# Optimization experiments

Measured on AMD Instinct MI355X. Metric: run time of the kernel, lower is better.

The kernel has to match this reference:

```python
import jax, jax.numpy as jnp
import numpy as np

E, D_IN, H1, H2 = 10, 784, 256, 64


def setup_inputs() -> dict:
    key = jax.random.key(0)
    ks = jax.random.split(key, 11)
    s = lambda fan_in: 1.0 / np.sqrt(fan_in)
    return {
        "x": jax.random.normal(ks[0], (65536, D_IN), dtype=jnp.float32),
        # stacked expert weights (E experts of Linear layers)
        "W1": jax.random.uniform(ks[1], (E, D_IN, H1), jnp.float32, -s(D_IN), s(D_IN)),
        "b1": jax.random.uniform(ks[2], (E, H1), jnp.float32, -s(D_IN), s(D_IN)),
        "W2": jax.random.uniform(ks[3], (E, H1, H2), jnp.float32, -s(H1), s(H1)),
        "b2": jax.random.uniform(ks[4], (E, H2), jnp.float32, -s(H1), s(H1)),
        "W3": jax.random.uniform(ks[5], (E, H2), jnp.float32, -s(H2), s(H2)),  # [E,64,1] squeezed
        "b3": jax.random.uniform(ks[6], (E,), jnp.float32, -s(H2), s(H2)),
        # gate: 784 -> 256 -> E
        "Wg1": jax.random.uniform(ks[7], (D_IN, H1), jnp.float32, -s(D_IN), s(D_IN)),
        "bg1": jax.random.uniform(ks[8], (H1,), jnp.float32, -s(D_IN), s(D_IN)),
        "Wg2": jax.random.uniform(ks[9], (H1, E), jnp.float32, -s(H1), s(H1)),
        "bg2": jax.random.uniform(ks[10], (E,), jnp.float32, -s(H1), s(H1)),
    }


def reference(x, W1, b1, W2, b2, W3, b3, Wg1, bg1, Wg2, bg2):
    # dense all-experts MLP stack, batched over experts as grouped GEMMs
    h = jax.nn.relu(jnp.einsum("bi,eih->beh", x, W1) + b1)        # [B,E,256]
    h = jax.nn.relu(jnp.einsum("beh,ehk->bek", h, W2) + b2)        # [B,E,64]
    expert_outputs = jnp.einsum("bek,ek->be", h, W3) + b3          # [B,E]
    g = jax.nn.relu(x @ Wg1 + bg1)
    gate_scores = jax.nn.softmax(g @ Wg2 + bg2, axis=-1)           # [B,E]
    output = gate_scores * expert_outputs                          # [B,E]
    return (output, gate_scores, expert_outputs)
```

## Files before the change

kernel.cpp:

```cpp
#include <hip/hip_runtime.h>
#include <hip/hip_bf16.h>
#include <stdint.h>

#define BTOT   65536
#define DIN    784
#define NH1    256
#define NH2    64
#define NEXP   10
#define BM     256
#define NKS1   25

#define SLOT(s)   (lds + (s) * 32768)
#define EXPL_OFF  131072
#define B2S_OFF   141312
#define W3S_OFF   143872
#define B3S_OFF   146432
#define BG2S_OFF  146496
#define LDS_TOTAL 146560

typedef short s16x8  __attribute__((ext_vector_type(8)));
typedef float f32x4  __attribute__((ext_vector_type(4)));
typedef float f32x16 __attribute__((ext_vector_type(16)));

__device__ __forceinline__ short bf16b(float v) {
    __bf16 b = (__bf16)v;
    return __builtin_bit_cast(short, b);
}

__device__ __forceinline__ void g2l16(const void* g, void* l) {
    __builtin_amdgcn_global_load_lds(
        (const __attribute__((address_space(1))) unsigned char*)g,
        (__attribute__((address_space(3))) unsigned char*)l, 16, 0, 0);
}

__global__ void prep_w1(const float* __restrict__ W1, const float* __restrict__ b1,
                        const float* __restrict__ Wg1, const float* __restrict__ bg1,
                        __bf16* __restrict__ dst) {
    int t = blockIdx.x * 256 + threadIdx.x;
    int lane = t & 63;
    int kh = (t >> 6) & 1;
    int nb = (t >> 7) & 7;
    int r  = t >> 10;
    int ks = r % 25, e = r / 25;
    int n  = nb * 32 + (lane & 31);
    int k0 = ks * 32 + kh * 16 + (lane >> 5) * 8;
    const float* src  = (e < NEXP) ? (W1 + (size_t)e * DIN * NH1) : Wg1;
    const float* bias = (e < NEXP) ? (b1 + e * NH1) : bg1;
    s16x8 o;
    #pragma unroll
    for (int j = 0; j < 8; ++j) {
        int k = k0 + j;
        float v = (k < DIN) ? src[(size_t)k * NH1 + n]
                            : ((k == DIN) ? bias[n] : 0.f);
        o[j] = bf16b(v);
    }
    *(s16x8*)((short*)dst + (size_t)t * 8) = o;
}

__global__ void prep_w2(const float* __restrict__ W2, __bf16* __restrict__ dst) {
    int t = blockIdx.x * 256 + threadIdx.x;
    int lane = t & 63;
    int kh = (t >> 6) & 1;
    int ks = (t >> 7) & 7;
    int jb = (t >> 10) & 1;
    int e  = t >> 11;
    int n  = jb * 32 + (lane & 31);
    int k0 = ks * 32 + kh * 16 + (lane >> 5) * 8;
    s16x8 o;
    #pragma unroll
    for (int j = 0; j < 8; ++j)
        o[j] = bf16b(W2[((size_t)e * NH1 + k0 + j) * NH2 + n]);
    *(s16x8*)((short*)dst + (size_t)t * 8) = o;
}

__global__ void prep_wg2(const float* __restrict__ Wg2, __bf16* __restrict__ dst) {
    int t = blockIdx.x * 256 + threadIdx.x;
    if (t >= 1024) return;
    int lane = t & 63;
    int kh = (t >> 6) & 1;
    int ks = t >> 7;
    int n  = lane & 31;
    int k0 = ks * 32 + kh * 16 + (lane >> 5) * 8;
    s16x8 o;
    #pragma unroll
    for (int j = 0; j < 8; ++j)
        o[j] = bf16b((n < NEXP) ? Wg2[(size_t)(k0 + j) * NEXP + n] : 0.f);
    *(s16x8*)((short*)dst + (size_t)t * 8) = o;
}

__global__ void prep_x(const float* __restrict__ x, __bf16* __restrict__ dst) {
    __shared__ short xl[32 * 800];
    const int rb = blockIdx.x >> 3, mq = blockIdx.x & 7;
    const int tid = threadIdx.x;
    const float* xg = x + ((size_t)rb * 256 + mq * 32) * DIN;
    #pragma unroll 4
    for (int i = 0; i < 25; ++i) {
        int idx = tid + i * 256;
        if (idx < 6272) {
            int r = idx / 196, c = (idx % 196) * 4;
            float4 v = *(const float4*)(xg + (size_t)r * DIN + c);
            uint2 w; short* p = (short*)&w;
            p[0] = bf16b(v.x); p[1] = bf16b(v.y);
            p[2] = bf16b(v.z); p[3] = bf16b(v.w);
            *(uint2*)(xl + r * 800 + c) = w;
        }
    }
    for (int i = tid; i < 32 * 16; i += 256) {
        int r = i >> 4, k = DIN + (i & 15);
        xl[r * 800 + k] = (k == DIN) ? bf16b(1.f) : (short)0;
    }
    __syncthreads();
    #pragma unroll 2
    for (int i = 0; i < 13; ++i) {
        int idx = tid + i * 256;
        if (idx < 3200) {
            int row = idx & 31, c8 = idx >> 5;
            int ks = c8 >> 2, rem = c8 & 3;
            int kh = rem >> 1, hw = rem & 1;
            s16x8 v = *(const s16x8*)(xl + row * 800 + ks * 32 + kh * 16 + hw * 8);
            *(s16x8*)((char*)dst + (((size_t)(rb * 25 + ks) * 8 + mq) * 2048)
                      + kh * 1024 + hw * 512 + row * 16) = v;
        }
    }
}

#define STAGE(S, E, KS) {                                                     \
        const char* xs_ = xtc + ((size_t)(KS) << 14) + tid * 16;              \
        char* xd_ = SLOT(S) + tid * 16;                                       \
        g2l16(xs_, xd_); g2l16(xs_ + 8192, xd_ + 8192);                       \
        const char* ws_ = w1c + (((size_t)(E) * 25 + (KS)) << 14) + tid * 16; \
        char* wd_ = SLOT(S) + 16384 + tid * 16;                               \
        g2l16(ws_, wd_); g2l16(ws_ + 8192, wd_ + 8192); }

#define COMPUTE(S) {                                                          \
        const char* ab = SLOT(S) + mw * 4096 + lane * 16;                     \
        const char* wb = SLOT(S) + 16384 + nw * 8192 + lane * 16;             \
        s16x8 xv[2][2], wv[4][2];                                             \
        _Pragma("unroll") for (int mt = 0; mt < 2; ++mt)                      \
            _Pragma("unroll") for (int kh = 0; kh < 2; ++kh)                  \
                xv[mt][kh] = *(const s16x8*)(ab + (mt * 2 + kh) * 1024);      \
        _Pragma("unroll") for (int nt = 0; nt < 4; ++nt)                      \
            _Pragma("unroll") for (int kh = 0; kh < 2; ++kh)                  \
                wv[nt][kh] = *(const s16x8*)(wb + (nt * 2 + kh) * 1024);      \
        _Pragma("unroll") for (int kh = 0; kh < 2; ++kh)                      \
            _Pragma("unroll") for (int nt = 0; nt < 4; ++nt)                  \
                _Pragma("unroll") for (int mt = 0; mt < 2; ++mt)              \
                    acc[nt][mt] = __builtin_amdgcn_mfma_f32_32x32x16_bf16(    \
                        wv[nt][kh], xv[mt][kh], acc[nt][mt], 0, 0, 0); }

#define RING_SYNC(VN) {                                                       \
        asm volatile("s_waitcnt vmcnt(" #VN ")" ::: "memory");                \
        __builtin_amdgcn_s_barrier();                                         \
        asm volatile("" ::: "memory"); }

#define BODY(S, KS) {                                                         \
        RING_SYNC(8)                                                          \
        COMPUTE(S)                                                            \
        STAGE(((S) + 3) & 3, e, (KS) + 3) }

__global__ void __launch_bounds__(512)
__attribute__((amdgpu_waves_per_eu(2, 2)))
moe_fused(const __bf16* __restrict__ xt, const float* __restrict__ b2g,
          const float* __restrict__ W3, const float* __restrict__ b3,
          const float* __restrict__ bg2, const __bf16* __restrict__ w1t,
          const __bf16* __restrict__ w2t, const __bf16* __restrict__ wg2t,
          float* __restrict__ out)
{
    extern __shared__ char lds[];
    char*  hb   = lds;
    float* expl = (float*)(lds + EXPL_OFF);
    float* b2s  = (float*)(lds + B2S_OFF);
    float* w3s  = (float*)(lds + W3S_OFF);
    float* b3s  = (float*)(lds + B3S_OFF);
    float* bg2s = (float*)(lds + BG2S_OFF);

    const int tid  = threadIdx.x;
    const int lane = tid & 63;
    const int wave = tid >> 6;
    const int rl   = lane & 31;
    const int hi   = lane >> 5;
    const int mw   = wave >> 1;
    const int nw   = wave & 1;
    const int row0 = blockIdx.x * BM;
    const char* w1c = (const char*)w1t;
    const char* w2c = (const char*)w2t;
    const char* wgc = (const char*)wg2t;
    const char* xtc = (const char*)xt + ((size_t)blockIdx.x * 25 << 14);

    for (int i = tid; i < NEXP * NH2; i += 512) { b2s[i] = b2g[i]; w3s[i] = W3[i]; }
    if (tid < NEXP) { b3s[tid] = b3[tid]; bg2s[tid] = bg2[tid]; }
    __syncthreads();

    f32x16 acc[4][2];

    #pragma unroll 1
    for (int e = 0; e <= NEXP; ++e) {
        #pragma unroll
        for (int nt = 0; nt < 4; ++nt)
            #pragma unroll
            for (int mt = 0; mt < 2; ++mt)
                #pragma unroll
                for (int q = 0; q < 16; ++q) acc[nt][mt][q] = 0.f;

        STAGE(0, e, 0)
        STAGE(1, e, 1)
        STAGE(2, e, 2)

        #pragma unroll 1
        for (int T = 0; T < 5; ++T) {
            const int k4 = 4 * T;
            BODY(0, k4)
            BODY(1, k4 + 1)
            BODY(2, k4 + 2)
            BODY(3, k4 + 3)
        }
        BODY(0, 20)
        BODY(1, 21)
        RING_SYNC(8)  COMPUTE(2)
        RING_SYNC(4)  COMPUTE(3)
        RING_SYNC(0)  COMPUTE(0)
        __syncthreads();

        #pragma unroll
        for (int mt = 0; mt < 2; ++mt)
            #pragma unroll
            for (int nt = 0; nt < 4; ++nt)
                #pragma unroll
                for (int q = 0; q < 4; ++q) {
                    uint2 wvv; short* p = (short*)&wvv;
                    #pragma unroll
                    for (int r2 = 0; r2 < 4; ++r2)
                        p[r2] = bf16b(fmaxf(acc[nt][mt][q * 4 + r2], 0.f));
                    *(uint2*)(hb + (((mw * 2 + mt) * 8 + (nw * 4 + nt)) * 2
                                    + (q >> 1)) * 1024
                                 + (q & 1) * 512 + rl * 16 + hi * 8) = wvv;
                }
        __syncthreads();

        if (e < NEXP) {
            f32x16 acc2[2];
            #pragma unroll
            for (int q = 0; q < 16; ++q) { acc2[0][q] = 0.f; acc2[1][q] = 0.f; }
            #pragma unroll
            for (int jb = 0; jb < 2; ++jb)
                #pragma unroll
                for (int k2 = 0; k2 < 8; ++k2)
                    #pragma unroll
                    for (int kh = 0; kh < 2; ++kh) {
                        s16x8 hf = *(const s16x8*)(hb + ((wave * 8 + k2) * 2 + kh) * 1024
                                                   + lane * 16);
                        s16x8 wf = *(const s16x8*)(w2c
                            + ((((size_t)e * 2 + jb) * 8 + k2) * 2 + kh) * 1024
                            + lane * 16);
                        acc2[jb] = __builtin_amdgcn_mfma_f32_32x32x16_bf16(
                            wf, hf, acc2[jb], 0, 0, 0);
                    }
            float part = 0.f;
            #pragma unroll
            for (int jb = 0; jb < 2; ++jb)
                #pragma unroll
                for (int q = 0; q < 4; ++q) {
                    f32x4 b2v = *(const f32x4*)(b2s + e * NH2 + jb * 32 + 8 * q + 4 * hi);
                    f32x4 w3v = *(const f32x4*)(w3s + e * NH2 + jb * 32 + 8 * q + 4 * hi);
                    #pragma unroll
                    for (int r2 = 0; r2 < 4; ++r2)
                        part += fmaxf(acc2[jb][q * 4 + r2] + b2v[r2], 0.f) * w3v[r2];
                }
            part += __shfl_xor(part, 32, 64);
            if (hi == 0)
                expl[(wave * 32 + rl) * NEXP + e] = part + b3s[e];
        } else {
            f32x16 acc3;
            #pragma unroll
            for (int q = 0; q < 16; ++q) acc3[q] = 0.f;
            #pragma unroll
            for (int k2 = 0; k2 < 8; ++k2)
                #pragma unroll
                for (int kh = 0; kh < 2; ++kh) {
                    s16x8 hf = *(const s16x8*)(hb + ((wave * 8 + k2) * 2 + kh) * 1024
                                               + lane * 16);
                    s16x8 gf = *(const s16x8*)(wgc + (k2 * 2 + kh) * 1024 + lane * 16);
                    acc3 = __builtin_amdgcn_mfma_f32_32x32x16_bf16(
                        gf, hf, acc3, 0, 0, 0);
                }
            const int m = wave * 32 + rl;
            float lv[16], mx = -1e30f;
            #pragma unroll
            for (int q = 0; q < 4; ++q)
                #pragma unroll
                for (int r2 = 0; r2 < 4; ++r2) {
                    int j = r2 + 8 * q + 4 * hi;
                    int rg = q * 4 + r2;
                    lv[rg] = (j < NEXP) ? (acc3[rg] + bg2s[j]) : -1e30f;
                    mx = fmaxf(mx, lv[rg]);
                }
            mx = fmaxf(mx, __shfl_xor(mx, 32, 64));
            float s = 0.f, pv[16];
            #pragma unroll
            for (int rg = 0; rg < 16; ++rg) {
                pv[rg] = (lv[rg] > -1e29f) ? __expf(lv[rg] - mx) : 0.f;
                s += pv[rg];
            }
            s += __shfl_xor(s, 32, 64);
            const float inv = 1.f / s;
            #pragma unroll
            for (int q = 0; q < 4; ++q)
                #pragma unroll
                for (int r2 = 0; r2 < 4; ++r2) {
                    int j = r2 + 8 * q + 4 * hi;
                    if (j < NEXP) {
                        float g  = pv[q * 4 + r2] * inv;
                        float eo = expl[m * NEXP + j];
                        size_t o = (size_t)(row0 + m) * NEXP + j;
                        out[o] = g * eo;
                        out[(size_t)BTOT * NEXP + o] = g;
                        out[(size_t)2 * BTOT * NEXP + o] = eo;
                    }
                }
        }
        __syncthreads();
    }
}

extern "C" void kernel_launch(void* const* d_in, const int* in_sizes, int n_in,
                              void* d_out, int out_size, void* d_ws, size_t ws_size,
                              hipStream_t stream) {
    (void)in_sizes; (void)n_in; (void)out_size; (void)ws_size;
    const float* x   = (const float*)d_in[0];
    const float* W1  = (const float*)d_in[1];
    const float* b1  = (const float*)d_in[2];
    const float* W2  = (const float*)d_in[3];
    const float* b2  = (const float*)d_in[4];
    const float* W3  = (const float*)d_in[5];
    const float* b3  = (const float*)d_in[6];
    const float* Wg1 = (const float*)d_in[7];
    const float* bg1 = (const float*)d_in[8];
    const float* Wg2 = (const float*)d_in[9];
    const float* bg2 = (const float*)d_in[10];

    __bf16* w1t  = (__bf16*)d_ws;
    __bf16* w2t  = w1t + (size_t)11 * 25 * 8192;
    __bf16* wg2t = w2t + (size_t)20480 * 8;
    __bf16* xt   = wg2t + (size_t)1024 * 8;

    hipFuncSetAttribute((const void*)moe_fused,
                        hipFuncAttributeMaxDynamicSharedMemorySize, LDS_TOTAL);

    prep_w1<<<1100, 256, 0, stream>>>(W1, b1, Wg1, bg1, w1t);
    prep_w2<<<80, 256, 0, stream>>>(W2, w2t);
    prep_wg2<<<4, 256, 0, stream>>>(Wg2, wg2t);
    prep_x<<<2048, 256, 0, stream>>>(x, xt);
    moe_fused<<<BTOT / BM, 512, LDS_TOTAL, stream>>>(
        xt, b2, W3, b3, bg2, w1t, w2t, wg2t, (float*)d_out);
}
```

Baseline: 347.9 us.

## Fuse x fp32-to-bf16 conversion into first expert pass of fused MoE kernel

Removes the separate prep_x kernel. During the first pass (e==0), each thread loads fp32 x rows directly, converts them to bf16, writes them into the LDS tile, and also stores them to the global xt buffer so later expert passes can reuse the converted tiles. The goal is to save one kernel launch and the extra global read/write round trip of x. The cost is that the first pass uses a simpler double-buffered pipeline with a full barrier every k-step, and register pressure from the 16-float staging array may hurt that pass.

```diff
diff --git a/kernel.cpp b/kernel.cpp
--- a/kernel.cpp
+++ b/kernel.cpp
@@ -88,42 +88,6 @@
     *(s16x8*)((short*)dst + (size_t)t * 8) = o;
 }
 
-__global__ void prep_x(const float* __restrict__ x, __bf16* __restrict__ dst) {
-    __shared__ short xl[32 * 800];
-    const int rb = blockIdx.x >> 3, mq = blockIdx.x & 7;
-    const int tid = threadIdx.x;
-    const float* xg = x + ((size_t)rb * 256 + mq * 32) * DIN;
-    #pragma unroll 4
-    for (int i = 0; i < 25; ++i) {
-        int idx = tid + i * 256;
-        if (idx < 6272) {
-            int r = idx / 196, c = (idx % 196) * 4;
-            float4 v = *(const float4*)(xg + (size_t)r * DIN + c);
-            uint2 w; short* p = (short*)&w;
-            p[0] = bf16b(v.x); p[1] = bf16b(v.y);
-            p[2] = bf16b(v.z); p[3] = bf16b(v.w);
-            *(uint2*)(xl + r * 800 + c) = w;
-        }
-    }
-    for (int i = tid; i < 32 * 16; i += 256) {
-        int r = i >> 4, k = DIN + (i & 15);
-        xl[r * 800 + k] = (k == DIN) ? bf16b(1.f) : (short)0;
-    }
-    __syncthreads();
-    #pragma unroll 2
-    for (int i = 0; i < 13; ++i) {
-        int idx = tid + i * 256;
-        if (idx < 3200) {
-            int row = idx & 31, c8 = idx >> 5;
-            int ks = c8 >> 2, rem = c8 & 3;
-            int kh = rem >> 1, hw = rem & 1;
-            s16x8 v = *(const s16x8*)(xl + row * 800 + ks * 32 + kh * 16 + hw * 8);
-            *(s16x8*)((char*)dst + (((size_t)(rb * 25 + ks) * 8 + mq) * 2048)
-                      + kh * 1024 + hw * 512 + row * 16) = v;
-        }
-    }
-}
-
 #define STAGE(S, E, KS) {                                                     \
         const char* xs_ = xtc + ((size_t)(KS) << 14) + tid * 16;              \
         char* xd_ = SLOT(S) + tid * 16;                                       \
@@ -131,6 +95,27 @@
         const char* ws_ = w1c + (((size_t)(E) * 25 + (KS)) << 14) + tid * 16; \
         char* wd_ = SLOT(S) + 16384 + tid * 16;                               \
         g2l16(ws_, wd_); g2l16(ws_ + 8192, wd_ + 8192); }
+
+#define WSTAGE1(S, KS) {                                                      \
+        const char* ws_ = w1c + ((size_t)(KS) << 14) + tid * 16;              \
+        char* wd_ = SLOT(S) + 16384 + tid * 16;                               \
+        g2l16(ws_, wd_); g2l16(ws_ + 8192, wd_ + 8192); }
+
+#define XLOAD(KS) { if ((KS) < 24 || xkh == 0) {                              \
+            _Pragma("unroll") for (int i4 = 0; i4 < 4; ++i4)                  \
+                *(float4*)(xf + 4 * i4) =                                     \
+                    *(const float4*)(xrp + (KS) * 32 + 4 * i4);               \
+        } else { _Pragma("unroll") for (int i4 = 0; i4 < 16; ++i4)            \
+                     xf[i4] = 0.f;                                            \
+                 xf[0] = 1.f; } }
+
+#define XWRITE(B, KS) { s16x8 l8, h8;                                         \
+        _Pragma("unroll") for (int j = 0; j < 8; ++j) {                       \
+            l8[j] = bf16b(xf[j]); h8[j] = bf16b(xf[8 + j]); }                 \
+        *(s16x8*)(SLOT(B) + xoff)       = l8;                                 \
+        *(s16x8*)(SLOT(B) + xoff + 512) = h8;                                 \
+        char* xg_ = xtw + ((size_t)(KS) << 14) + xoff;                        \
+        *(s16x8*)xg_ = l8; *(s16x8*)(xg_ + 512) = h8; }
 
 #define COMPUTE(S) {                                                          \
         const char* ab = SLOT(S) + mw * 4096 + lane * 16;                     \
@@ -160,11 +145,11 @@
 
 __global__ void __launch_bounds__(512)
 __attribute__((amdgpu_waves_per_eu(2, 2)))
-moe_fused(const __bf16* __restrict__ xt, const float* __restrict__ b2g,
-          const float* __restrict__ W3, const float* __restrict__ b3,
-          const float* __restrict__ bg2, const __bf16* __restrict__ w1t,
-          const __bf16* __restrict__ w2t, const __bf16* __restrict__ wg2t,
-          float* __restrict__ out)
+moe_fused(const float* __restrict__ x, __bf16* __restrict__ xt,
+          const float* __restrict__ b2g, const float* __restrict__ W3,
+          const float* __restrict__ b3, const float* __restrict__ bg2,
+          const __bf16* __restrict__ w1t, const __bf16* __restrict__ w2t,
+          const __bf16* __restrict__ wg2t, float* __restrict__ out)
 {
     extern __shared__ char lds[];
     char*  hb   = lds;
@@ -186,6 +171,12 @@
     const char* w2c = (const char*)w2t;
     const char* wgc = (const char*)wg2t;
     const char* xtc = (const char*)xt + ((size_t)blockIdx.x * 25 << 14);
+    char*       xtw = (char*)xt + ((size_t)blockIdx.x * 25 << 14);
+
+    const int xrow = tid >> 1, xkh = tid & 1;
+    const float* xrp = x + (size_t)(row0 + xrow) * DIN + xkh * 16;
+    const int xoff = ((xrow >> 5) * 2 + xkh) * 1024 + (xrow & 31) * 16;
+    float xf[16];
 
     for (int i = tid; i < NEXP * NH2; i += 512) { b2s[i] = b2g[i]; w3s[i] = W3[i]; }
     if (tid < NEXP) { b3s[tid] = b3[tid]; bg2s[tid] = bg2[tid]; }
@@ -202,24 +193,39 @@
                 #pragma unroll
                 for (int q = 0; q < 16; ++q) acc[nt][mt][q] = 0.f;
 
-        STAGE(0, e, 0)
-        STAGE(1, e, 1)
-        STAGE(2, e, 2)
-
-        #pragma unroll 1
-        for (int T = 0; T < 5; ++T) {
-            const int k4 = 4 * T;
-            BODY(0, k4)
-            BODY(1, k4 + 1)
-            BODY(2, k4 + 2)
-            BODY(3, k4 + 3)
+        if (e == 0) {
+            int cur = 0;
+            XLOAD(0)
+            WSTAGE1(0, 0)
+            XWRITE(0, 0)
+            __syncthreads();
+            #pragma unroll 1
+            for (int ks = 0; ks < NKS1; ++ks) {
+                if (ks < 24) { XLOAD(ks + 1) WSTAGE1(cur ^ 1, ks + 1) }
+                COMPUTE(cur)
+                if (ks < 24) XWRITE(cur ^ 1, ks + 1)
+                __syncthreads();
+                cur ^= 1;
+            }
+        } else {
+            STAGE(0, e, 0)
+            STAGE(1, e, 1)
+            STAGE(2, e, 2)
+            #pragma unroll 1
+            for (int T = 0; T < 5; ++T) {
+                const int k4 = 4 * T;
+                BODY(0, k4)
+                BODY(1, k4 + 1)
+                BODY(2, k4 + 2)
+                BODY(3, k4 + 3)
+            }
+            BODY(0, 20)
+            BODY(1, 21)
+            RING_SYNC(8)  COMPUTE(2)
+            RING_SYNC(4)  COMPUTE(3)
+            RING_SYNC(0)  COMPUTE(0)
+            __syncthreads();
         }
-        BODY(0, 20)
-        BODY(1, 21)
-        RING_SYNC(8)  COMPUTE(2)
-        RING_SYNC(4)  COMPUTE(3)
-        RING_SYNC(0)  COMPUTE(0)
-        __syncthreads();
 
         #pragma unroll
         for (int mt = 0; mt < 2; ++mt)
@@ -349,7 +355,6 @@
     prep_w1<<<1100, 256, 0, stream>>>(W1, b1, Wg1, bg1, w1t);
     prep_w2<<<80, 256, 0, stream>>>(W2, w2t);
     prep_wg2<<<4, 256, 0, stream>>>(Wg2, wg2t);
-    prep_x<<<2048, 256, 0, stream>>>(x, xt);
     moe_fused<<<BTOT / BM, 512, LDS_TOTAL, stream>>>(
-        xt, b2, W3, b3, bg2, w1t, w2t, wg2t, (float*)d_out);
-}
+        x, xt, b2, W3, b3, bg2, w1t, w2t, wg2t, (float*)d_out);
+}
```

After: 329.1 us. 5.4% less time.
